# Kernel tuning notes

Hardware: AMD Instinct MI355X
Metric: run time of the kernel (lower is better)

## Reference

```python
import jax, jax.numpy as jnp
import numpy as np

BS, T, ND, DS, IN, H = 512, 100, 10, 6, 256, 256
SA = IN * ND + H  # 2816, attention MLP width


def setup_inputs() -> dict:
    key = jax.random.key(0)
    ks = jax.random.split(key, 8)
    def lin(k, out_d, in_d):
        return jax.random.normal(k, (out_d, in_d), jnp.float32) * (1.0 / np.sqrt(in_d)).astype(np.float32)
    return {
        "descriptors": jax.random.normal(ks[0], (BS, T, ND, DS), jnp.float32),
        "Wd": lin(ks[1], IN, DS), "bd": jnp.zeros((IN,), jnp.float32),
        "W1": lin(ks[2], SA, SA), "b1": jnp.zeros((SA,), jnp.float32),
        "W2": lin(ks[3], IN, SA), "b2": jnp.zeros((IN,), jnp.float32),
        "Wv": lin(ks[4], ND, SA), "bv": jnp.zeros((ND,), jnp.float32),
        "W_ih": lin(ks[5], 4 * H, IN), "W_hh": lin(ks[6], 4 * H, H),
        "b_ih": jnp.zeros((4 * H,), jnp.float32), "b_hh": jnp.zeros((4 * H,), jnp.float32),
    }


def reference(descriptors, Wd, bd, W1, b1, W2, b2, Wv, bv, W_ih, W_hh, b_ih, b_hh):
    bs = descriptors.shape[0]
    dt = descriptors.dtype
    desc_tm = jnp.swapaxes(descriptors, 0, 1)  # [T, bs, ND, DS] time-major for scan
    h0 = jnp.zeros((bs, H), dt)
    c0 = jnp.zeros((bs, H), dt)
    inp0 = jnp.zeros((bs, IN), dt)

    def step(carry, d):
        h, c, inp = carry
        # torch.nn.LSTMCell: gate order i, f, g, o
        gates = inp @ W_ih.T + b_ih + h @ W_hh.T + b_hh  # [bs, 4H]
        i, f, g, o = jnp.split(gates, 4, axis=-1)
        c = jax.nn.sigmoid(f) * c + jax.nn.sigmoid(i) * jnp.tanh(g)
        h = jax.nn.sigmoid(o) * jnp.tanh(c)
        # FrameAttention
        emb = d @ Wd.T + bd                               # [bs, ND, IN]
        x = jnp.concatenate([emb.reshape(bs, ND * IN), h], axis=-1)  # [bs, SA]
        x = jax.nn.relu(x @ W1.T + b1)
        nxt = jax.nn.relu(x @ W2.T + b2)
        a = x @ Wv.T + bv  # training mode: no sigmoid
        return (h, c, nxt), a

    _, att = jax.lax.scan(step, (h0, c0, inp0), desc_tm)  # att: [T, bs, ND]
    return jnp.swapaxes(att, 0, 1)  # [bs, T, ND]
```

## Files before the change

kernel.cpp:

```cpp
#include <hip/hip_runtime.h>
#include <hip/hip_bf16.h>
#include <math.h>

#define TT 100
#define ND 10
#define DS 6
#define SAW 2816

typedef _Float16 half8 __attribute__((ext_vector_type(8)));
typedef float floatx4 __attribute__((ext_vector_type(4)));

__device__ __forceinline__ void gload_lds16(const _Float16* g, _Float16* l) {
    __builtin_amdgcn_global_load_lds((const __attribute__((address_space(1))) void*)g,
                                     (__attribute__((address_space(3))) void*)l, 16, 0, 0);
}

__global__ __launch_bounds__(256) void gemm_big(
    const _Float16* __restrict__ Ah, const _Float16* __restrict__ Al, int lda,
    const _Float16* __restrict__ Bh, const _Float16* __restrict__ Bl, int ldb,
    float* __restrict__ Cpart, size_t zstride, int ldc, int Kloc)
{
    __shared__ alignas(16) _Float16 lds[4 * 128 * 32];

    const int tid = threadIdx.x;
    const int w = tid >> 6, l = tid & 63;
    const int m0 = blockIdx.x * 128, n0 = blockIdx.y * 128;
    const int koff = blockIdx.z * Kloc;

    const _Float16* plane_src;
    int plane_ld;
    if (w == 0)      { plane_src = Ah + (size_t)m0 * lda; plane_ld = lda; }
    else if (w == 1) { plane_src = Al + (size_t)m0 * lda; plane_ld = lda; }
    else if (w == 2) { plane_src = Bh + (size_t)n0 * ldb; plane_ld = ldb; }
    else             { plane_src = Bl + (size_t)n0 * ldb; plane_ld = ldb; }
    const int srow_in_chunk = l >> 2;
    const int scol = (l & 3) * 8;
    _Float16* const lds_plane = lds + w * 4096;

    const int wr = (w >> 1) * 64, wc = (w & 1) * 64;
    const int fr = l & 15, fk = (l >> 4) * 8;

    floatx4 acc[4][4];
    const floatx4 z4 = {0.f, 0.f, 0.f, 0.f};
#pragma unroll
    for (int i = 0; i < 4; ++i)
#pragma unroll
        for (int j = 0; j < 4; ++j) acc[i][j] = z4;

    for (int kt = 0; kt < Kloc; kt += 32) {
        __syncthreads();
#pragma unroll
        for (int i = 0; i < 8; ++i) {
            const int row = i * 16 + srow_in_chunk;
            gload_lds16(plane_src + (size_t)row * plane_ld + koff + kt + scol,
                        lds_plane + i * 512);
        }
        __syncthreads();

        half8 aH[4], aL[4], bH[4], bL[4];
#pragma unroll
        for (int f = 0; f < 4; ++f) {
            const int ra = (wr + f * 16 + fr) * 32 + fk;
            const int rb = (wc + f * 16 + fr) * 32 + fk;
            aH[f] = *(const half8*)&lds[ra];
            aL[f] = *(const half8*)&lds[4096 + ra];
            bH[f] = *(const half8*)&lds[8192 + rb];
            bL[f] = *(const half8*)&lds[12288 + rb];
        }
#pragma unroll
        for (int mf = 0; mf < 4; ++mf)
#pragma unroll
            for (int nf = 0; nf < 4; ++nf)
                acc[mf][nf] = __builtin_amdgcn_mfma_f32_16x16x32_f16(aH[mf], bH[nf], acc[mf][nf], 0, 0, 0);
#pragma unroll
        for (int mf = 0; mf < 4; ++mf)
#pragma unroll
            for (int nf = 0; nf < 4; ++nf)
                acc[mf][nf] = __builtin_amdgcn_mfma_f32_16x16x32_f16(aH[mf], bL[nf], acc[mf][nf], 0, 0, 0);
#pragma unroll
        for (int mf = 0; mf < 4; ++mf)
#pragma unroll
            for (int nf = 0; nf < 4; ++nf)
                acc[mf][nf] = __builtin_amdgcn_mfma_f32_16x16x32_f16(aL[mf], bH[nf], acc[mf][nf], 0, 0, 0);
    }

    float* const Cz = Cpart + (size_t)blockIdx.z * zstride;
    const int cr = (l >> 4) * 4, cc = l & 15;
#pragma unroll
    for (int mf = 0; mf < 4; ++mf) {
        const int row = m0 + wr + mf * 16 + cr;
#pragma unroll
        for (int nf = 0; nf < 4; ++nf) {
            const int col = n0 + wc + nf * 16 + cc;
#pragma unroll
            for (int r = 0; r < 4; ++r)
                Cz[(size_t)(row + r) * ldc + col] = acc[mf][nf][r];
        }
    }
}

__global__ __launch_bounds__(256) void gemm_s16_part(
    const _Float16* __restrict__ Ah, const _Float16* __restrict__ Al, int lda,
    const _Float16* __restrict__ Bh, const _Float16* __restrict__ Bl, int ldb,
    float* __restrict__ Cf, int ldc, int Kloc)
{
    __shared__ alignas(16) _Float16 sAh[64 * 32];
    __shared__ alignas(16) _Float16 sAl[64 * 32];
    __shared__ alignas(16) _Float16 sBh[64 * 32];
    __shared__ alignas(16) _Float16 sBl[64 * 32];

    const int tid = threadIdx.x;
    const int w = tid >> 6, l = tid & 63;
    const int m0 = blockIdx.x * 64, n0 = blockIdx.y * 64;
    const int koff = blockIdx.z * Kloc;

    const int sr = 16 * w + (l >> 2);
    const int sc = (l & 3) * 8;
    const int sidx = sr * 32 + sc;
    const _Float16* gAh = Ah + (size_t)(m0 + sr) * lda + koff + sc;
    const _Float16* gAl = Al + (size_t)(m0 + sr) * lda + koff + sc;
    const _Float16* gBh = Bh + (size_t)(n0 + sr) * ldb + koff + sc;
    const _Float16* gBl = Bl + (size_t)(n0 + sr) * ldb + koff + sc;

    const int mw = (w >> 1) * 32, nw = (w & 1) * 32;
    const int fr = l & 15, fk = (l >> 4) * 8;

    floatx4 acc[2][2];
    const floatx4 z = {0.f, 0.f, 0.f, 0.f};
#pragma unroll
    for (int i = 0; i < 2; ++i)
#pragma unroll
        for (int j = 0; j < 2; ++j) acc[i][j] = z;

    half8 rAh = *(const half8*)gAh;
    half8 rAl = *(const half8*)gAl;
    half8 rBh = *(const half8*)gBh;
    half8 rBl = *(const half8*)gBl;

    for (int kt = 0; kt < Kloc; kt += 32) {
        *(half8*)&sAh[sidx] = rAh;
        *(half8*)&sAl[sidx] = rAl;
        *(half8*)&sBh[sidx] = rBh;
        *(half8*)&sBl[sidx] = rBl;
        __syncthreads();
        if (kt + 32 < Kloc) {
            rAh = *(const half8*)(gAh + kt + 32);
            rAl = *(const half8*)(gAl + kt + 32);
            rBh = *(const half8*)(gBh + kt + 32);
            rBl = *(const half8*)(gBl + kt + 32);
        }
        half8 aH[2], aL[2], bH[2], bL[2];
#pragma unroll
        for (int mf = 0; mf < 2; ++mf) {
            const int ro = (mw + mf * 16 + fr) * 32 + fk;
            aH[mf] = *(const half8*)&sAh[ro];
            aL[mf] = *(const half8*)&sAl[ro];
        }
#pragma unroll
        for (int nf = 0; nf < 2; ++nf) {
            const int ro = (nw + nf * 16 + fr) * 32 + fk;
            bH[nf] = *(const half8*)&sBh[ro];
            bL[nf] = *(const half8*)&sBl[ro];
        }
#pragma unroll
        for (int mf = 0; mf < 2; ++mf)
#pragma unroll
            for (int nf = 0; nf < 2; ++nf)
                acc[mf][nf] = __builtin_amdgcn_mfma_f32_16x16x32_f16(aH[mf], bH[nf], acc[mf][nf], 0, 0, 0);
#pragma unroll
        for (int mf = 0; mf < 2; ++mf)
#pragma unroll
            for (int nf = 0; nf < 2; ++nf)
                acc[mf][nf] = __builtin_amdgcn_mfma_f32_16x16x32_f16(aH[mf], bL[nf], acc[mf][nf], 0, 0, 0);
#pragma unroll
        for (int mf = 0; mf < 2; ++mf)
#pragma unroll
            for (int nf = 0; nf < 2; ++nf)
                acc[mf][nf] = __builtin_amdgcn_mfma_f32_16x16x32_f16(aL[mf], bH[nf], acc[mf][nf], 0, 0, 0);
        __syncthreads();
    }

    const int cr = (l >> 4) * 4, cc = l & 15;
#pragma unroll
    for (int nf = 0; nf < 2; ++nf) {
        const int col = n0 + nw + nf * 16 + cc;
#pragma unroll
        for (int mf = 0; mf < 2; ++mf) {
            const int row = m0 + mw + mf * 16 + cr;
#pragma unroll
            for (int r = 0; r < 4; ++r)
                Cf[(size_t)blockIdx.z * (512 * 256) + (size_t)(row + r) * ldc + col]
                    = acc[mf][nf][r];
        }
    }
}

__global__ __launch_bounds__(256) void yred(const float* __restrict__ pbufY,
                                            const float* __restrict__ b1,
                                            _Float16* __restrict__ yhi,
                                            _Float16* __restrict__ ylo)
{
    const int b = blockIdx.x, tid = threadIdx.x;
    for (int i = tid; i < SAW; i += 256) {
        float s = b1[i];
#pragma unroll
        for (int z = 0; z < 4; ++z) s += pbufY[(size_t)z * 1441792 + (size_t)b * SAW + i];
        s = s > 0.f ? s : 0.f;
        const _Float16 h = (_Float16)s;
        yhi[(size_t)b * SAW + i] = h;
        ylo[(size_t)b * SAW + i] = (_Float16)(s - (float)h);
    }
}

__global__ __launch_bounds__(256) void lstm_emb(
    const float* __restrict__ gpart, const float* __restrict__ b_ih,
    const float* __restrict__ b_hh, float* __restrict__ cbuf,
    _Float16* __restrict__ zhi, _Float16* __restrict__ zlo,
    _Float16* __restrict__ xhi, _Float16* __restrict__ xlo,
    const float* __restrict__ desc, const float* __restrict__ Wd,
    const float* __restrict__ bd, int t)
{
    __shared__ float sd[60];
    __shared__ float swd[1536];
    const int b = blockIdx.x, k = threadIdx.x;
    if (k < 60) sd[k] = desc[(size_t)b * (TT * ND * DS) + t * (ND * DS) + k];
    for (int i = k; i < 1536; i += 256) swd[i] = Wd[i];

    float gate[4];
#pragma unroll
    for (int g = 0; g < 4; ++g) {
        const int idx = g * 256 + k;
        float s = b_ih[idx] + b_hh[idx];
#pragma unroll
        for (int z = 0; z < 4; ++z) s += gpart[z * 524288 + b * 1024 + idx];
        gate[g] = s;
    }
    const float si = 1.f / (1.f + expf(-gate[0]));
    const float sf = 1.f / (1.f + expf(-gate[1]));
    const float so = 1.f / (1.f + expf(-gate[3]));
    float cv = cbuf[b * 256 + k];
    cv = sf * cv + si * tanhf(gate[2]);
    const float hv = so * tanhf(cv);
    cbuf[b * 256 + k] = cv;
    {
        const _Float16 h = (_Float16)hv;
        const _Float16 lo = (_Float16)(hv - (float)h);
        zhi[b * 512 + 256 + k] = h;   zlo[b * 512 + 256 + k] = lo;
        xhi[(size_t)b * SAW + 2560 + k] = h;
        xlo[(size_t)b * SAW + 2560 + k] = lo;
    }
    __syncthreads();

    const float bdv = bd[k];
#pragma unroll
    for (int n = 0; n < ND; ++n) {
        float a = bdv;
#pragma unroll
        for (int d = 0; d < DS; ++d) a += sd[n * DS + d] * swd[k * DS + d];
        const _Float16 h = (_Float16)a;
        xhi[(size_t)b * SAW + n * 256 + k] = h;
        xlo[(size_t)b * SAW + n * 256 + k] = (_Float16)(a - (float)h);
    }
}

__global__ __launch_bounds__(256) void av_w2fin(
    const _Float16* __restrict__ yhi, const _Float16* __restrict__ ylo,
    const float* __restrict__ Wv, const float* __restrict__ bv,
    const float* __restrict__ pbuf, const float* __restrict__ b2,
    _Float16* __restrict__ zhi, _Float16* __restrict__ zlo,
    float* __restrict__ out, int t)
{
    __shared__ float ys[SAW];
    __shared__ float red[ND][4];
    const int b = blockIdx.x, tid = threadIdx.x;
    for (int i = tid; i < SAW; i += 256)
        ys[i] = (float)yhi[(size_t)b * SAW + i] + (float)ylo[(size_t)b * SAW + i];
    __syncthreads();

    float pacc[ND];
#pragma unroll
    for (int n = 0; n < ND; ++n) pacc[n] = 0.f;
    for (int kk = tid; kk < SAW; kk += 256) {
        const float yv = ys[kk];
#pragma unroll
        for (int n = 0; n < ND; ++n) pacc[n] += yv * Wv[n * SAW + kk];
    }
    const int lane = tid & 63, wid = tid >> 6;
#pragma unroll
    for (int n = 0; n < ND; ++n) {
        float v = pacc[n];
        for (int off = 32; off > 0; off >>= 1) v += __shfl_down(v, off, 64);
        if (lane == 0) red[n][wid] = v;
    }
    {
        const int j = tid;
        float s = b2[j];
#pragma unroll
        for (int kc = 0; kc < 4; ++kc) s += pbuf[kc * 131072 + b * 256 + j];
        s = s > 0.f ? s : 0.f;
        const _Float16 h = (_Float16)s;
        zhi[b * 512 + j] = h;
        zlo[b * 512 + j] = (_Float16)(s - (float)h);
    }
    __syncthreads();
    if (tid < ND) {
        const float s = red[tid][0] + red[tid][1] + red[tid][2] + red[tid][3] + bv[tid];
        out[(size_t)b * (TT * ND) + t * ND + tid] = s;
    }
}

__global__ void build_wcat_split(const float* __restrict__ W_ih, const float* __restrict__ W_hh,
                                 _Float16* __restrict__ wchi, _Float16* __restrict__ wclo)
{
    const int j = blockIdx.x, k = threadIdx.x;
    const float v1 = W_ih[j * 256 + k];
    const _Float16 h1 = (_Float16)v1;
    wchi[j * 512 + k] = h1;
    wclo[j * 512 + k] = (_Float16)(v1 - (float)h1);
    const float v2 = W_hh[j * 256 + k];
    const _Float16 h2 = (_Float16)v2;
    wchi[j * 512 + 256 + k] = h2;
    wclo[j * 512 + 256 + k] = (_Float16)(v2 - (float)h2);
}

__global__ __launch_bounds__(256) void cvt_hilo(const float* __restrict__ src,
                                                _Float16* __restrict__ hi,
                                                _Float16* __restrict__ lo, int n)
{
    int i = blockIdx.x * 256 + threadIdx.x;
    const int stride = gridDim.x * 256;
    for (; i < n; i += stride) {
        const float v = src[i];
        const _Float16 h = (_Float16)v;
        hi[i] = h;
        lo[i] = (_Float16)(v - (float)h);
    }
}

extern "C" void kernel_launch(void* const* d_in, const int* in_sizes, int n_in,
                              void* d_out, int out_size, void* d_ws, size_t ws_size,
                              hipStream_t stream)
{
    const float* desc = (const float*)d_in[0];
    const float* Wd   = (const float*)d_in[1];
    const float* bd   = (const float*)d_in[2];
    const float* W1   = (const float*)d_in[3];
    const float* b1   = (const float*)d_in[4];
    const float* W2   = (const float*)d_in[5];
    const float* b2   = (const float*)d_in[6];
    const float* Wv   = (const float*)d_in[7];
    const float* bv   = (const float*)d_in[8];
    const float* W_ih = (const float*)d_in[9];
    const float* W_hh = (const float*)d_in[10];
    const float* b_ih = (const float*)d_in[11];
    const float* b_hh = (const float*)d_in[12];
    float* out = (float*)d_out;

    char* ws = (char*)d_ws;
    _Float16* zhi  = (_Float16*)(ws);
    _Float16* zlo  = (_Float16*)(ws + 524288);
    float*    cbuf = (float*)(ws + 1048576);
    _Float16* xhi  = (_Float16*)(ws + 1572864);
    _Float16* xlo  = (_Float16*)(ws + 4456448);
    _Float16* yhi  = xhi;
    _Float16* ylo  = xlo;
    float*    gpart = (float*)(ws + 7340032);
    float*    pbufY = (float*)(ws + 7340032);
    float*    pbufW2= (float*)(ws + 7340032);
    _Float16* wchi = (_Float16*)(ws + 30408704);
    _Float16* wclo = (_Float16*)(ws + 31457280);
    _Float16* w2hi = (_Float16*)(ws + 32505856);
    _Float16* w2lo = (_Float16*)(ws + 33947648);
    _Float16* w1hi = (_Float16*)(ws + 35389440);
    _Float16* w1lo = (_Float16*)(ws + 51249152);

    hipMemsetAsync(ws, 0, 1572864, stream);
    build_wcat_split<<<dim3(1024), dim3(256), 0, stream>>>(W_ih, W_hh, wchi, wclo);
    cvt_hilo<<<dim3(4096), dim3(256), 0, stream>>>(W1, w1hi, w1lo, SAW * SAW);
    cvt_hilo<<<dim3(704), dim3(256), 0, stream>>>(W2, w2hi, w2lo, 256 * SAW);

    for (int t = 0; t < TT; ++t) {
        gemm_big<<<dim3(4, 8, 4), dim3(256), 0, stream>>>(
            zhi, zlo, 512, wchi, wclo, 512, gpart, 524288, 1024, 128);
        lstm_emb<<<dim3(512), dim3(256), 0, stream>>>(gpart, b_ih, b_hh, cbuf,
                                                      zhi, zlo, xhi, xlo,
                                                      desc, Wd, bd, t);
        gemm_big<<<dim3(4, 22, 4), dim3(256), 0, stream>>>(
            xhi, xlo, SAW, w1hi, w1lo, SAW, pbufY, 1441792, SAW, 704);
        yred<<<dim3(512), dim3(256), 0, stream>>>(pbufY, b1, yhi, ylo);
        gemm_s16_part<<<dim3(8, 4, 4), dim3(256), 0, stream>>>(
            yhi, ylo, SAW, w2hi, w2lo, SAW, pbufW2, 256, 704);
        av_w2fin<<<dim3(512), dim3(256), 0, stream>>>(yhi, ylo, Wv, bv, pbufW2, b2,
                                                      zhi, zlo, out, t);
    }
}
```

Measured before the change: 8.738 ms.

## Pipeline GEMM with double-buffered LDS, fuse W1 epilogue, fold Wv into W2 GEMM

Replaces the 256-thread GEMM with a 512-thread version. It double-buffers LDS tiles through async global-to-LDS loads, with explicit vmcnt waits and barriers. The W1 GEMM drops split-K and applies bias, ReLU and the hi/lo fp16 split in its epilogue, which removes the yred kernel and its traffic over the partial-sum buffer. Wv is appended as extra rows to the W2 weight matrix, so the attention output comes out of the same GEMM and av_fin becomes a simple reduction. The risk is that the W1 GEMM now launches only 88 blocks with four times the K length each, which leaves many compute units idle.

Result: slower. 10.33 ms (+18.2%).

```diff
diff --git a/kernel.cpp b/kernel.cpp
--- a/kernel.cpp
+++ b/kernel.cpp
@@ -15,122 +15,151 @@
                                      (__attribute__((address_space(3))) void*)l, 16, 0, 0);
 }
 
-__global__ __launch_bounds__(256) void gemm_big(
+template<int EPI>
+__global__ __launch_bounds__(512) void gemm_pipe(
     const _Float16* __restrict__ Ah, const _Float16* __restrict__ Al, int lda,
     const _Float16* __restrict__ Bh, const _Float16* __restrict__ Bl, int ldb,
-    float* __restrict__ Cpart, size_t zstride, int ldc, int Kloc)
-{
-    __shared__ alignas(16) _Float16 lds[4 * 128 * 32];
+    const float* __restrict__ bias,
+    float* __restrict__ Cf, size_t zstride,
+    _Float16* __restrict__ Chi, _Float16* __restrict__ Clo,
+    int ldc, int Kloc)
+{
+    __shared__ alignas(16) _Float16 lds[2][4][4096];
 
     const int tid = threadIdx.x;
     const int w = tid >> 6, l = tid & 63;
     const int m0 = blockIdx.x * 128, n0 = blockIdx.y * 128;
     const int koff = blockIdx.z * Kloc;
 
-    const _Float16* plane_src;
-    int plane_ld;
-    if (w == 0)      { plane_src = Ah + (size_t)m0 * lda; plane_ld = lda; }
-    else if (w == 1) { plane_src = Al + (size_t)m0 * lda; plane_ld = lda; }
-    else if (w == 2) { plane_src = Bh + (size_t)n0 * ldb; plane_ld = ldb; }
-    else             { plane_src = Bl + (size_t)n0 * ldb; plane_ld = ldb; }
-    const int srow_in_chunk = l >> 2;
+    const int plane = w >> 1;
+    const _Float16* psrc;
+    int pld;
+    if (plane == 0)      { psrc = Ah + (size_t)m0 * lda; pld = lda; }
+    else if (plane == 1) { psrc = Al + (size_t)m0 * lda; pld = lda; }
+    else if (plane == 2) { psrc = Bh + (size_t)n0 * ldb; pld = ldb; }
+    else                 { psrc = Bl + (size_t)n0 * ldb; pld = ldb; }
+    const int srow0 = (w & 1) * 64 + (l >> 2);
     const int scol = (l & 3) * 8;
-    _Float16* const lds_plane = lds + w * 4096;
-
-    const int wr = (w >> 1) * 64, wc = (w & 1) * 64;
+    const int chnk0 = (w & 1) * 4;
+
+    const int wr = (w >> 2) * 64, wc = (w & 3) * 32;
     const int fr = l & 15, fk = (l >> 4) * 8;
 
-    floatx4 acc[4][4];
+    floatx4 acc[4][2];
     const floatx4 z4 = {0.f, 0.f, 0.f, 0.f};
 #pragma unroll
     for (int i = 0; i < 4; ++i)
 #pragma unroll
-        for (int j = 0; j < 4; ++j) acc[i][j] = z4;
-
+        for (int j = 0; j < 2; ++j) acc[i][j] = z4;
+
+#define STAGE(buf, kg)                                                          \
+    {                                                                           \
+        _Float16* const db = &lds[buf][plane][0];                               \
+        _Pragma("unroll")                                                       \
+        for (int i = 0; i < 4; ++i) {                                           \
+            const int row = srow0 + i * 16;                                     \
+            gload_lds16(psrc + (size_t)row * pld + (kg) + scol,                 \
+                        db + (chnk0 + i) * 512);                                \
+        }                                                                       \
+    }
+
+    STAGE(0, koff);
+    int cur = 0;
     for (int kt = 0; kt < Kloc; kt += 32) {
-        __syncthreads();
-#pragma unroll
-        for (int i = 0; i < 8; ++i) {
-            const int row = i * 16 + srow_in_chunk;
-            gload_lds16(plane_src + (size_t)row * plane_ld + koff + kt + scol,
-                        lds_plane + i * 512);
-        }
-        __syncthreads();
-
-        half8 aH[4], aL[4], bH[4], bL[4];
-#pragma unroll
-        for (int f = 0; f < 4; ++f) {
-            const int ra = (wr + f * 16 + fr) * 32 + fk;
-            const int rb = (wc + f * 16 + fr) * 32 + fk;
-            aH[f] = *(const half8*)&lds[ra];
-            aL[f] = *(const half8*)&lds[4096 + ra];
-            bH[f] = *(const half8*)&lds[8192 + rb];
-            bL[f] = *(const half8*)&lds[12288 + rb];
+        asm volatile("s_barrier" ::: "memory");
+        if (kt + 32 < Kloc) {
+            STAGE(cur ^ 1, koff + kt + 32);
+            asm volatile("s_waitcnt vmcnt(4)" ::: "memory");
+        } else {
+            asm volatile("s_waitcnt vmcnt(0)" ::: "memory");
+        }
+        asm volatile("s_barrier" ::: "memory");
+
+        half8 aH[4], aL[4], bH[2], bL[2];
+#pragma unroll
+        for (int mf = 0; mf < 4; ++mf) {
+            const int ro = (wr + mf * 16 + fr) * 32 + fk;
+            aH[mf] = *(const half8*)&lds[cur][0][ro];
+            aL[mf] = *(const half8*)&lds[cur][1][ro];
+        }
+#pragma unroll
+        for (int nf = 0; nf < 2; ++nf) {
+            const int ro = (wc + nf * 16 + fr) * 32 + fk;
+            bH[nf] = *(const half8*)&lds[cur][2][ro];
+            bL[nf] = *(const half8*)&lds[cur][3][ro];
         }
 #pragma unroll
         for (int mf = 0; mf < 4; ++mf)
 #pragma unroll
-            for (int nf = 0; nf < 4; ++nf)
+            for (int nf = 0; nf < 2; ++nf)
                 acc[mf][nf] = __builtin_amdgcn_mfma_f32_16x16x32_f16(aH[mf], bH[nf], acc[mf][nf], 0, 0, 0);
 #pragma unroll
         for (int mf = 0; mf < 4; ++mf)
 #pragma unroll
-            for (int nf = 0; nf < 4; ++nf)
+            for (int nf = 0; nf < 2; ++nf)
                 acc[mf][nf] = __builtin_amdgcn_mfma_f32_16x16x32_f16(aH[mf], bL[nf], acc[mf][nf], 0, 0, 0);
 #pragma unroll
         for (int mf = 0; mf < 4; ++mf)
 #pragma unroll
-            for (int nf = 0; nf < 4; ++nf)
+            for (int nf = 0; nf < 2; ++nf)
                 acc[mf][nf] = __builtin_amdgcn_mfma_f32_16x16x32_f16(aL[mf], bH[nf], acc[mf][nf], 0, 0, 0);
-    }
-
-    float* const Cz = Cpart + (size_t)blockIdx.z * zstride;
+        cur ^= 1;
+    }
+#undef STAGE
+
     const int cr = (l >> 4) * 4, cc = l & 15;
 #pragma unroll
     for (int mf = 0; mf < 4; ++mf) {
         const int row = m0 + wr + mf * 16 + cr;
 #pragma unroll
-        for (int nf = 0; nf < 4; ++nf) {
+        for (int nf = 0; nf < 2; ++nf) {
             const int col = n0 + wc + nf * 16 + cc;
 #pragma unroll
-            for (int r = 0; r < 4; ++r)
-                Cz[(size_t)(row + r) * ldc + col] = acc[mf][nf][r];
-        }
-    }
-}
-
-__global__ __launch_bounds__(256) void gemm_s16_part(
-    const _Float16* __restrict__ Ah, const _Float16* __restrict__ Al, int lda,
-    const _Float16* __restrict__ Bh, const _Float16* __restrict__ Bl, int ldb,
-    float* __restrict__ Cf, int ldc, int Kloc)
+            for (int r = 0; r < 4; ++r) {
+                float v = acc[mf][nf][r];
+                if constexpr (EPI == 0) {
+                    Cf[(size_t)blockIdx.z * zstride + (size_t)(row + r) * ldc + col] = v;
+                } else {
+                    v += bias[col];
+                    v = v > 0.f ? v : 0.f;
+                    const _Float16 h = (_Float16)v;
+                    Chi[(size_t)(row + r) * ldc + col] = h;
+                    Clo[(size_t)(row + r) * ldc + col] = (_Float16)(v - (float)h);
+                }
+            }
+        }
+    }
+}
+
+__global__ __launch_bounds__(256) void gemm_w2v(
+    const _Float16* __restrict__ Ah, const _Float16* __restrict__ Al,
+    const _Float16* __restrict__ Bh, const _Float16* __restrict__ Bl,
+    float* __restrict__ Cf, int Kloc)
 {
     __shared__ alignas(16) _Float16 sAh[64 * 32];
     __shared__ alignas(16) _Float16 sAl[64 * 32];
     __shared__ alignas(16) _Float16 sBh[64 * 32];
     __shared__ alignas(16) _Float16 sBl[64 * 32];
 
-    const int tid = threadIdx.x;
-    const int w = tid >> 6, l = tid & 63;
+    const int tid = threadIdx.x, w = tid >> 6, l = tid & 63;
     const int m0 = blockIdx.x * 64, n0 = blockIdx.y * 64;
     const int koff = blockIdx.z * Kloc;
 
-    const int sr = 16 * w + (l >> 2);
-    const int sc = (l & 3) * 8;
-    const int sidx = sr * 32 + sc;
-    const _Float16* gAh = Ah + (size_t)(m0 + sr) * lda + koff + sc;
-    const _Float16* gAl = Al + (size_t)(m0 + sr) * lda + koff + sc;
-    const _Float16* gBh = Bh + (size_t)(n0 + sr) * ldb + koff + sc;
-    const _Float16* gBl = Bl + (size_t)(n0 + sr) * ldb + koff + sc;
+    const int sr = 16 * w + (l >> 2), sc = (l & 3) * 8, sidx = sr * 32 + sc;
+    const _Float16* gAh = Ah + (size_t)(m0 + sr) * SAW + koff + sc;
+    const _Float16* gAl = Al + (size_t)(m0 + sr) * SAW + koff + sc;
+    const _Float16* gBh = Bh + (size_t)(n0 + sr) * SAW + koff + sc;
+    const _Float16* gBl = Bl + (size_t)(n0 + sr) * SAW + koff + sc;
 
     const int mw = (w >> 1) * 32, nw = (w & 1) * 32;
     const int fr = l & 15, fk = (l >> 4) * 8;
 
     floatx4 acc[2][2];
-    const floatx4 z = {0.f, 0.f, 0.f, 0.f};
+    const floatx4 z4 = {0.f, 0.f, 0.f, 0.f};
 #pragma unroll
     for (int i = 0; i < 2; ++i)
 #pragma unroll
-        for (int j = 0; j < 2; ++j) acc[i][j] = z;
+        for (int j = 0; j < 2; ++j) acc[i][j] = z4;
 
     half8 rAh = *(const half8*)gAh;
     half8 rAl = *(const half8*)gAl;
@@ -189,26 +218,9 @@
             const int row = m0 + mw + mf * 16 + cr;
 #pragma unroll
             for (int r = 0; r < 4; ++r)
-                Cf[(size_t)blockIdx.z * (512 * 256) + (size_t)(row + r) * ldc + col]
+                Cf[(size_t)blockIdx.z * 163840 + (size_t)(row + r) * 320 + col]
                     = acc[mf][nf][r];
         }
-    }
-}
-
-__global__ __launch_bounds__(256) void yred(const float* __restrict__ pbufY,
-                                            const float* __restrict__ b1,
-                                            _Float16* __restrict__ yhi,
-                                            _Float16* __restrict__ ylo)
-{
-    const int b = blockIdx.x, tid = threadIdx.x;
-    for (int i = tid; i < SAW; i += 256) {
-        float s = b1[i];
-#pragma unroll
-        for (int z = 0; z < 4; ++z) s += pbufY[(size_t)z * 1441792 + (size_t)b * SAW + i];
-        s = s > 0.f ? s : 0.f;
-        const _Float16 h = (_Float16)s;
-        yhi[(size_t)b * SAW + i] = h;
-        ylo[(size_t)b * SAW + i] = (_Float16)(s - (float)h);
     }
 }
 
@@ -263,54 +275,31 @@
     }
 }
 
-__global__ __launch_bounds__(256) void av_w2fin(
-    const _Float16* __restrict__ yhi, const _Float16* __restrict__ ylo,
-    const float* __restrict__ Wv, const float* __restrict__ bv,
+__global__ __launch_bounds__(256) void av_fin(
     const float* __restrict__ pbuf, const float* __restrict__ b2,
+    const float* __restrict__ bv,
     _Float16* __restrict__ zhi, _Float16* __restrict__ zlo,
     float* __restrict__ out, int t)
 {
-    __shared__ float ys[SAW];
-    __shared__ float red[ND][4];
-    const int b = blockIdx.x, tid = threadIdx.x;
-    for (int i = tid; i < SAW; i += 256)
-        ys[i] = (float)yhi[(size_t)b * SAW + i] + (float)ylo[(size_t)b * SAW + i];
-    __syncthreads();
-
-    float pacc[ND];
-#pragma unroll
-    for (int n = 0; n < ND; ++n) pacc[n] = 0.f;
-    for (int kk = tid; kk < SAW; kk += 256) {
-        const float yv = ys[kk];
-#pragma unroll
-        for (int n = 0; n < ND; ++n) pacc[n] += yv * Wv[n * SAW + kk];
-    }
-    const int lane = tid & 63, wid = tid >> 6;
-#pragma unroll
-    for (int n = 0; n < ND; ++n) {
-        float v = pacc[n];
-        for (int off = 32; off > 0; off >>= 1) v += __shfl_down(v, off, 64);
-        if (lane == 0) red[n][wid] = v;
-    }
-    {
-        const int j = tid;
-        float s = b2[j];
-#pragma unroll
-        for (int kc = 0; kc < 4; ++kc) s += pbuf[kc * 131072 + b * 256 + j];
-        s = s > 0.f ? s : 0.f;
-        const _Float16 h = (_Float16)s;
-        zhi[b * 512 + j] = h;
-        zlo[b * 512 + j] = (_Float16)(s - (float)h);
-    }
-    __syncthreads();
-    if (tid < ND) {
-        const float s = red[tid][0] + red[tid][1] + red[tid][2] + red[tid][3] + bv[tid];
-        out[(size_t)b * (TT * ND) + t * ND + tid] = s;
+    const int b = blockIdx.x, j = threadIdx.x;
+    float s = b2[j];
+#pragma unroll
+    for (int z = 0; z < 4; ++z) s += pbuf[z * 163840 + b * 320 + j];
+    s = s > 0.f ? s : 0.f;
+    const _Float16 h = (_Float16)s;
+    zhi[b * 512 + j] = h;
+    zlo[b * 512 + j] = (_Float16)(s - (float)h);
+    if (j < ND) {
+        float s2 = bv[j];
+#pragma unroll
+        for (int z = 0; z < 4; ++z) s2 += pbuf[z * 163840 + b * 320 + 256 + j];
+        out[(size_t)b * (TT * ND) + t * ND + j] = s2;
     }
 }
 
 __global__ void build_wcat_split(const float* __restrict__ W_ih, const float* __restrict__ W_hh,
-                                 _Float16* __restrict__ wchi, _Float16* __restrict__ wclo)
+                                 _Float16* __restrict__ wchi, _Float16* __restrict__ wclo,
+                                 float* __restrict__ bcat)
 {
     const int j = blockIdx.x, k = threadIdx.x;
     const float v1 = W_ih[j * 256 + k];
@@ -321,6 +310,23 @@
     const _Float16 h2 = (_Float16)v2;
     wchi[j * 512 + 256 + k] = h2;
     wclo[j * 512 + 256 + k] = (_Float16)(v2 - (float)h2);
+    if (k == 0) bcat[j] = 0.f;
+}
+
+__global__ __launch_bounds__(256) void build_w2v(const float* __restrict__ W2,
+                                                 const float* __restrict__ Wv,
+                                                 _Float16* __restrict__ hi,
+                                                 _Float16* __restrict__ lo)
+{
+    const int j = blockIdx.x;
+    for (int k = threadIdx.x; k < SAW; k += 256) {
+        float v = 0.f;
+        if (j < 256)       v = W2[(size_t)j * SAW + k];
+        else if (j < 266)  v = Wv[(size_t)(j - 256) * SAW + k];
+        const _Float16 h = (_Float16)v;
+        hi[(size_t)j * SAW + k] = h;
+        lo[(size_t)j * SAW + k] = (_Float16)(v - (float)h);
+    }
 }
 
 __global__ __launch_bounds__(256) void cvt_hilo(const float* __restrict__ src,
@@ -357,40 +363,40 @@
     float* out = (float*)d_out;
 
     char* ws = (char*)d_ws;
-    _Float16* zhi  = (_Float16*)(ws);
-    _Float16* zlo  = (_Float16*)(ws + 524288);
-    float*    cbuf = (float*)(ws + 1048576);
-    _Float16* xhi  = (_Float16*)(ws + 1572864);
-    _Float16* xlo  = (_Float16*)(ws + 4456448);
-    _Float16* yhi  = xhi;
-    _Float16* ylo  = xlo;
+    _Float16* zhi   = (_Float16*)(ws);
+    _Float16* zlo   = (_Float16*)(ws + 524288);
+    float*    cbuf  = (float*)(ws + 1048576);
+    _Float16* xhi   = (_Float16*)(ws + 1572864);
+    _Float16* xlo   = (_Float16*)(ws + 4456448);
     float*    gpart = (float*)(ws + 7340032);
-    float*    pbufY = (float*)(ws + 7340032);
-    float*    pbufW2= (float*)(ws + 7340032);
-    _Float16* wchi = (_Float16*)(ws + 30408704);
-    _Float16* wclo = (_Float16*)(ws + 31457280);
-    _Float16* w2hi = (_Float16*)(ws + 32505856);
-    _Float16* w2lo = (_Float16*)(ws + 33947648);
-    _Float16* w1hi = (_Float16*)(ws + 35389440);
-    _Float16* w1lo = (_Float16*)(ws + 51249152);
+    float*    pbufW2= (float*)(ws + 15728640);
+    _Float16* yhi   = (_Float16*)(ws + 18350080);
+    _Float16* ylo   = (_Float16*)(ws + 21233664);
+    _Float16* wchi  = (_Float16*)(ws + 24117248);
+    _Float16* wclo  = (_Float16*)(ws + 25165824);
+    _Float16* w2vhi = (_Float16*)(ws + 26214400);
+    _Float16* w2vlo = (_Float16*)(ws + 28016640);
+    _Float16* w1hi  = (_Float16*)(ws + 29818880);
+    _Float16* w1lo  = (_Float16*)(ws + 45678592);
+    float*    bcat  = (float*)(ws + 61538304);
 
     hipMemsetAsync(ws, 0, 1572864, stream);
-    build_wcat_split<<<dim3(1024), dim3(256), 0, stream>>>(W_ih, W_hh, wchi, wclo);
+    build_wcat_split<<<dim3(1024), dim3(256), 0, stream>>>(W_ih, W_hh, wchi, wclo, bcat);
+    build_w2v<<<dim3(320), dim3(256), 0, stream>>>(W2, Wv, w2vhi, w2vlo);
     cvt_hilo<<<dim3(4096), dim3(256), 0, stream>>>(W1, w1hi, w1lo, SAW * SAW);
-    cvt_hilo<<<dim3(704), dim3(256), 0, stream>>>(W2, w2hi, w2lo, 256 * SAW);
 
     for (int t = 0; t < TT; ++t) {
-        gemm_big<<<dim3(4, 8, 4), dim3(256), 0, stream>>>(
-            zhi, zlo, 512, wchi, wclo, 512, gpart, 524288, 1024, 128);
+        gemm_pipe<0><<<dim3(4, 8, 4), dim3(512), 0, stream>>>(
+            zhi, zlo, 512, wchi, wclo, 512, nullptr,
+            gpart, 524288, nullptr, nullptr, 1024, 128);
         lstm_emb<<<dim3(512), dim3(256), 0, stream>>>(gpart, b_ih, b_hh, cbuf,
                                                       zhi, zlo, xhi, xlo,
                                                       desc, Wd, bd, t);
-        gemm_big<<<dim3(4, 22, 4), dim3(256), 0, stream>>>(
-            xhi, xlo, SAW, w1hi, w1lo, SAW, pbufY, 1441792, SAW, 704);
-        yred<<<dim3(512), dim3(256), 0, stream>>>(pbufY, b1, yhi, ylo);
-        gemm_s16_part<<<dim3(8, 4, 4), dim3(256), 0, stream>>>(
-            yhi, ylo, SAW, w2hi, w2lo, SAW, pbufW2, 256, 704);
-        av_w2fin<<<dim3(512), dim3(256), 0, stream>>>(yhi, ylo, Wv, bv, pbufW2, b2,
-                                                      zhi, zlo, out, t);
-    }
-}
+        gemm_pipe<1><<<dim3(4, 22, 1), dim3(512), 0, stream>>>(
+            xhi, xlo, SAW, w1hi, w1lo, SAW, b1,
+            nullptr, 0, yhi, ylo, SAW, SAW);
+        gemm_w2v<<<dim3(8, 5, 4), dim3(256), 0, stream>>>(
+            yhi, ylo, w2vhi, w2vlo, pbufW2, 704);
+        av_fin<<<dim3(512), dim3(256), 0, stream>>>(pbufW2, b2, bv, zhi, zlo, out, t);
+    }
+}
```

## Double-buffer GEMM LDS loads, widen to 512 threads, and remap blocks for XCD locality

Applied to the files above, without the earlier changes.

Replaces the split-K GEMM kernel with a version that double-buffers its LDS tiles. The next K-slice is issued with global_load_lds before computing on the current one, using explicit vmcnt waits and barriers. The block grows to 8 waves, each computing a 64x32 sub-tile, so register pressure per wave drops and more waves are available to hide latency. Both GEMM kernels now launch on a 1D grid with a swizzled block index that spreads tiles across XCDs. The cost is twice the LDS use and hand-written waitcnt logic that must stay consistent with the number of loads in flight.

Result: faster. 8.234 ms (-5.8%).

```diff
diff --git a/kernel.cpp b/kernel.cpp
--- a/kernel.cpp
+++ b/kernel.cpp
@@ -15,86 +15,109 @@
                                      (__attribute__((address_space(3))) void*)l, 16, 0, 0);
 }
 
-__global__ __launch_bounds__(256) void gemm_big(
+__global__ __launch_bounds__(512) void gemm_pipe(
     const _Float16* __restrict__ Ah, const _Float16* __restrict__ Al, int lda,
     const _Float16* __restrict__ Bh, const _Float16* __restrict__ Bl, int ldb,
-    float* __restrict__ Cpart, size_t zstride, int ldc, int Kloc)
-{
-    __shared__ alignas(16) _Float16 lds[4 * 128 * 32];
+    float* __restrict__ Cf, size_t zstride, int ldc, int Kloc, int gm, int gn)
+{
+    __shared__ alignas(16) _Float16 lds[2][4][4096];
+
+    const int nwg = gridDim.x;
+    const int v = (blockIdx.x & 7) * (nwg >> 3) + (blockIdx.x >> 3);
+    const int m0 = (v % gm) * 128;
+    const int n0 = ((v / gm) % gn) * 128;
+    const int zb = v / (gm * gn);
+    const int koff = zb * Kloc;
 
     const int tid = threadIdx.x;
     const int w = tid >> 6, l = tid & 63;
-    const int m0 = blockIdx.x * 128, n0 = blockIdx.y * 128;
-    const int koff = blockIdx.z * Kloc;
-
-    const _Float16* plane_src;
-    int plane_ld;
-    if (w == 0)      { plane_src = Ah + (size_t)m0 * lda; plane_ld = lda; }
-    else if (w == 1) { plane_src = Al + (size_t)m0 * lda; plane_ld = lda; }
-    else if (w == 2) { plane_src = Bh + (size_t)n0 * ldb; plane_ld = ldb; }
-    else             { plane_src = Bl + (size_t)n0 * ldb; plane_ld = ldb; }
-    const int srow_in_chunk = l >> 2;
+
+    const int plane = w >> 1;
+    const _Float16* psrc;
+    int pld;
+    if (plane == 0)      { psrc = Ah + (size_t)m0 * lda; pld = lda; }
+    else if (plane == 1) { psrc = Al + (size_t)m0 * lda; pld = lda; }
+    else if (plane == 2) { psrc = Bh + (size_t)n0 * ldb; pld = ldb; }
+    else                 { psrc = Bl + (size_t)n0 * ldb; pld = ldb; }
+    const int srow0 = (w & 1) * 64 + (l >> 2);
     const int scol = (l & 3) * 8;
-    _Float16* const lds_plane = lds + w * 4096;
-
-    const int wr = (w >> 1) * 64, wc = (w & 1) * 64;
+    const int chnk0 = (w & 1) * 4;
+
+    const int wr = (w >> 2) * 64, wc = (w & 3) * 32;
     const int fr = l & 15, fk = (l >> 4) * 8;
 
-    floatx4 acc[4][4];
+    floatx4 acc[4][2];
     const floatx4 z4 = {0.f, 0.f, 0.f, 0.f};
 #pragma unroll
     for (int i = 0; i < 4; ++i)
 #pragma unroll
-        for (int j = 0; j < 4; ++j) acc[i][j] = z4;
-
+        for (int j = 0; j < 2; ++j) acc[i][j] = z4;
+
+#define STAGE(buf, kg)                                                          \
+    {                                                                           \
+        _Float16* const db = &lds[buf][plane][0];                               \
+        _Pragma("unroll")                                                       \
+        for (int i = 0; i < 4; ++i) {                                           \
+            const int row = srow0 + i * 16;                                     \
+            gload_lds16(psrc + (size_t)row * pld + (kg) + scol,                 \
+                        db + (chnk0 + i) * 512);                                \
+        }                                                                       \
+    }
+
+    STAGE(0, koff);
+    int cur = 0;
     for (int kt = 0; kt < Kloc; kt += 32) {
-        __syncthreads();
-#pragma unroll
-        for (int i = 0; i < 8; ++i) {
-            const int row = i * 16 + srow_in_chunk;
-            gload_lds16(plane_src + (size_t)row * plane_ld + koff + kt + scol,
-                        lds_plane + i * 512);
-        }
-        __syncthreads();
-
-        half8 aH[4], aL[4], bH[4], bL[4];
-#pragma unroll
-        for (int f = 0; f < 4; ++f) {
-            const int ra = (wr + f * 16 + fr) * 32 + fk;
-            const int rb = (wc + f * 16 + fr) * 32 + fk;
-            aH[f] = *(const half8*)&lds[ra];
-            aL[f] = *(const half8*)&lds[4096 + ra];
-            bH[f] = *(const half8*)&lds[8192 + rb];
-            bL[f] = *(const half8*)&lds[12288 + rb];
+        asm volatile("s_barrier" ::: "memory");
+        if (kt + 32 < Kloc) {
+            STAGE(cur ^ 1, koff + kt + 32);
+            asm volatile("s_waitcnt vmcnt(4)" ::: "memory");
+        } else {
+            asm volatile("s_waitcnt vmcnt(0)" ::: "memory");
+        }
+        asm volatile("s_barrier" ::: "memory");
+
+        half8 aH[4], aL[4], bH[2], bL[2];
+#pragma unroll
+        for (int mf = 0; mf < 4; ++mf) {
+            const int ro = (wr + mf * 16 + fr) * 32 + fk;
+            aH[mf] = *(const half8*)&lds[cur][0][ro];
+            aL[mf] = *(const half8*)&lds[cur][1][ro];
+        }
+#pragma unroll
+        for (int nf = 0; nf < 2; ++nf) {
+            const int ro = (wc + nf * 16 + fr) * 32 + fk;
+            bH[nf] = *(const half8*)&lds[cur][2][ro];
+            bL[nf] = *(const half8*)&lds[cur][3][ro];
         }
 #pragma unroll
         for (int mf = 0; mf < 4; ++mf)
 #pragma unroll
-            for (int nf = 0; nf < 4; ++nf)
+            for (int nf = 0; nf < 2; ++nf)
                 acc[mf][nf] = __builtin_amdgcn_mfma_f32_16x16x32_f16(aH[mf], bH[nf], acc[mf][nf], 0, 0, 0);
 #pragma unroll
         for (int mf = 0; mf < 4; ++mf)
 #pragma unroll
-            for (int nf = 0; nf < 4; ++nf)
+            for (int nf = 0; nf < 2; ++nf)
                 acc[mf][nf] = __builtin_amdgcn_mfma_f32_16x16x32_f16(aH[mf], bL[nf], acc[mf][nf], 0, 0, 0);
 #pragma unroll
         for (int mf = 0; mf < 4; ++mf)
 #pragma unroll
-            for (int nf = 0; nf < 4; ++nf)
+            for (int nf = 0; nf < 2; ++nf)
                 acc[mf][nf] = __builtin_amdgcn_mfma_f32_16x16x32_f16(aL[mf], bH[nf], acc[mf][nf], 0, 0, 0);
-    }
-
-    float* const Cz = Cpart + (size_t)blockIdx.z * zstride;
+        cur ^= 1;
+    }
+#undef STAGE
+
     const int cr = (l >> 4) * 4, cc = l & 15;
 #pragma unroll
     for (int mf = 0; mf < 4; ++mf) {
         const int row = m0 + wr + mf * 16 + cr;
 #pragma unroll
-        for (int nf = 0; nf < 4; ++nf) {
+        for (int nf = 0; nf < 2; ++nf) {
             const int col = n0 + wc + nf * 16 + cc;
 #pragma unroll
             for (int r = 0; r < 4; ++r)
-                Cz[(size_t)(row + r) * ldc + col] = acc[mf][nf][r];
+                Cf[(size_t)zb * zstride + (size_t)(row + r) * ldc + col] = acc[mf][nf][r];
         }
     }
 }
@@ -102,21 +125,22 @@
 __global__ __launch_bounds__(256) void gemm_s16_part(
     const _Float16* __restrict__ Ah, const _Float16* __restrict__ Al, int lda,
     const _Float16* __restrict__ Bh, const _Float16* __restrict__ Bl, int ldb,
-    float* __restrict__ Cf, int ldc, int Kloc)
+    float* __restrict__ Cf, int ldc, int Kloc, int gm, int gn)
 {
     __shared__ alignas(16) _Float16 sAh[64 * 32];
     __shared__ alignas(16) _Float16 sAl[64 * 32];
     __shared__ alignas(16) _Float16 sBh[64 * 32];
     __shared__ alignas(16) _Float16 sBl[64 * 32];
 
-    const int tid = threadIdx.x;
-    const int w = tid >> 6, l = tid & 63;
-    const int m0 = blockIdx.x * 64, n0 = blockIdx.y * 64;
-    const int koff = blockIdx.z * Kloc;
-
-    const int sr = 16 * w + (l >> 2);
-    const int sc = (l & 3) * 8;
-    const int sidx = sr * 32 + sc;
+    const int nwg = gridDim.x;
+    const int v = (blockIdx.x & 7) * (nwg >> 3) + (blockIdx.x >> 3);
+    const int m0 = (v % gm) * 64;
+    const int n0 = ((v / gm) % gn) * 64;
+    const int zb = v / (gm * gn);
+    const int koff = zb * Kloc;
+
+    const int tid = threadIdx.x, w = tid >> 6, l = tid & 63;
+    const int sr = 16 * w + (l >> 2), sc = (l & 3) * 8, sidx = sr * 32 + sc;
     const _Float16* gAh = Ah + (size_t)(m0 + sr) * lda + koff + sc;
     const _Float16* gAl = Al + (size_t)(m0 + sr) * lda + koff + sc;
     const _Float16* gBh = Bh + (size_t)(n0 + sr) * ldb + koff + sc;
@@ -126,11 +150,11 @@
     const int fr = l & 15, fk = (l >> 4) * 8;
 
     floatx4 acc[2][2];
-    const floatx4 z = {0.f, 0.f, 0.f, 0.f};
+    const floatx4 z4 = {0.f, 0.f, 0.f, 0.f};
 #pragma unroll
     for (int i = 0; i < 2; ++i)
 #pragma unroll
-        for (int j = 0; j < 2; ++j) acc[i][j] = z;
+        for (int j = 0; j < 2; ++j) acc[i][j] = z4;
 
     half8 rAh = *(const half8*)gAh;
     half8 rAl = *(const half8*)gAl;
@@ -189,7 +213,7 @@
             const int row = m0 + mw + mf * 16 + cr;
 #pragma unroll
             for (int r = 0; r < 4; ++r)
-                Cf[(size_t)blockIdx.z * (512 * 256) + (size_t)(row + r) * ldc + col]
+                Cf[(size_t)zb * (512 * 256) + (size_t)(row + r) * ldc + col]
                     = acc[mf][nf][r];
         }
     }
@@ -357,13 +381,13 @@
     float* out = (float*)d_out;
 
     char* ws = (char*)d_ws;
-    _Float16* zhi  = (_Float16*)(ws);
-    _Float16* zlo  = (_Float16*)(ws + 524288);
-    float*    cbuf = (float*)(ws + 1048576);
-    _Float16* xhi  = (_Float16*)(ws + 1572864);
-    _Float16* xlo  = (_Float16*)(ws + 4456448);
-    _Float16* yhi  = xhi;
-    _Float16* ylo  = xlo;
+    _Float16* zhi   = (_Float16*)(ws);
+    _Float16* zlo   = (_Float16*)(ws + 524288);
+    float*    cbuf  = (float*)(ws + 1048576);
+    _Float16* xhi   = (_Float16*)(ws + 1572864);
+    _Float16* xlo   = (_Float16*)(ws + 4456448);
+    _Float16* yhi   = xhi;
+    _Float16* ylo   = xlo;
     float*    gpart = (float*)(ws + 7340032);
     float*    pbufY = (float*)(ws + 7340032);
     float*    pbufW2= (float*)(ws + 7340032);
@@ -380,16 +404,16 @@
     cvt_hilo<<<dim3(704), dim3(256), 0, stream>>>(W2, w2hi, w2lo, 256 * SAW);
 
     for (int t = 0; t < TT; ++t) {
-        gemm_big<<<dim3(4, 8, 4), dim3(256), 0, stream>>>(
-            zhi, zlo, 512, wchi, wclo, 512, gpart, 524288, 1024, 128);
+        gemm_pipe<<<dim3(128), dim3(512), 0, stream>>>(
+            zhi, zlo, 512, wchi, wclo, 512, gpart, 524288, 1024, 128, 4, 8);
         lstm_emb<<<dim3(512), dim3(256), 0, stream>>>(gpart, b_ih, b_hh, cbuf,
                                                       zhi, zlo, xhi, xlo,
                                                       desc, Wd, bd, t);
-        gemm_big<<<dim3(4, 22, 4), dim3(256), 0, stream>>>(
-            xhi, xlo, SAW, w1hi, w1lo, SAW, pbufY, 1441792, SAW, 704);
+        gemm_pipe<<<dim3(352), dim3(512), 0, stream>>>(
+            xhi, xlo, SAW, w1hi, w1lo, SAW, pbufY, 1441792, SAW, 704, 4, 22);
         yred<<<dim3(512), dim3(256), 0, stream>>>(pbufY, b1, yhi, ylo);
-        gemm_s16_part<<<dim3(8, 4, 4), dim3(256), 0, stream>>>(
-            yhi, ylo, SAW, w2hi, w2lo, SAW, pbufW2, 256, 704);
+        gemm_s16_part<<<dim3(128), dim3(256), 0, stream>>>(
+            yhi, ylo, SAW, w2hi, w2lo, SAW, pbufW2, 256, 704, 8, 4);
         av_w2fin<<<dim3(512), dim3(256), 0, stream>>>(yhi, ylo, Wv, bv, pbufW2, b2,
                                                       zhi, zlo, out, t);
     }
```
